# Optimization experiments

Hardware: AMD Instinct MI355X
Metric: run time of the kernel (lower is better)

The kernel has to match this reference:

```python
import jax, jax.numpy as jnp
import numpy as np

ALPHA = 0.5

def pairwise_sqdist(a, b):
    # a: [B,N,3], b: [B,M,3] -> [B,N,M] squared euclidean distances
    a2 = jnp.sum(a * a, axis=-1)[:, :, None]
    b2 = jnp.sum(b * b, axis=-1)[:, None, :]
    ab = jnp.einsum('bnd,bmd->bnm', a, b)
    return jnp.maximum(a2 + b2 - 2.0 * ab, 0.0)

def setup_inputs() -> dict:
    key = jax.random.key(0)
    k1, k2, k3, k4, k5 = jax.random.split(key, 5)
    B, N_UP, N_SEED, N_GT, N_RAD = 4, 8192, 2048, 8192, 1024
    return {
        'pc_up':   jax.random.normal(k1, (B, N_UP, 3), dtype=jnp.float32),
        'pc_seed': jax.random.normal(k2, (B, N_SEED, 3), dtype=jnp.float32),
        'pc_conf': jax.random.uniform(k3, (B, N_RAD, 1), dtype=jnp.float32),
        'pc2':     jax.random.normal(k4, (B, N_GT, 3), dtype=jnp.float32),
        'pc3':     jax.random.normal(k5, (B, N_RAD, 3), dtype=jnp.float32),
    }

def reference(pc_up, pc_seed, pc_conf, pc2, pc3):
    # --- confidence score target: exp(-min euclidean dist from radar to GT) ---
    d_rad_gt = pairwise_sqdist(pc3, pc2)                      # [B,N_rad,N_gt]
    min_dist = jnp.sqrt(jnp.min(d_rad_gt, axis=-1))           # [B,N_rad]
    gt_scores = jnp.exp(-min_dist)[..., None]                 # [B,N_rad,1]
    conf_loss = jnp.mean((pc_conf - gt_scores) ** 2)

    # --- Chamfer (squared distances, as standard ChamferDistance kernels) ---
    d_up_gt = pairwise_sqdist(pc_up, pc2)                     # [B,N_up,N_gt]
    dist1 = jnp.min(d_up_gt, axis=2)                          # up -> gt
    dist2 = jnp.min(d_up_gt, axis=1)                          # gt -> up
    chamfer_up = 0.5 * jnp.mean(dist1) + 2.0 * jnp.mean(dist2)

    # --- EMD surrogate: nearest-neighbor matching cost, sqrt(dist).mean() ---
    # (original uses an approximate auction-based emdFunction; nearest-neighbor
    # assignment is the standard differentiable reference surrogate)
    emd_loss = jnp.mean(jnp.sqrt(dist1))

    final_loss = ALPHA * chamfer_up + ALPHA * conf_loss + emd_loss
    return final_loss
```

## Files before the change

### kernel.cpp

```cpp
#include <hip/hip_runtime.h>
#include <math.h>


#define THREADS 256
#define NSPLIT 16
#define COLS 512
#define NTILES (COLS / 32)

typedef __attribute__((ext_vector_type(8))) short s8v;
typedef __attribute__((ext_vector_type(16))) float f16v;

__device__ __forceinline__ unsigned short f2bf(float x) {
    unsigned u = __float_as_uint(x);
    u += 0x7FFFu + ((u >> 16) & 1u);
    return (unsigned short)(u >> 16);
}
__device__ __forceinline__ float bf2f(unsigned short h) {
    return __uint_as_float((unsigned)h << 16);
}

__global__ __launch_bounds__(THREADS, 4) void
mfma_pass_kernel(const float* __restrict__ pc_up, const float* __restrict__ pc2,
                 const float* __restrict__ pc3,
                 float* p1, float* p2, float* p3) {
    __shared__ unsigned short tiles[NTILES][2][32][8];

    int bid = blockIdx.x;
    const float* Ap;
    const float* Bp;
    float* part;
    int NA, rowsTot;
    if (bid < 1024) {
        Ap = pc_up; Bp = pc2; part = p1; NA = 8192; rowsTot = 32768;
    } else if (bid < 2048) {
        bid -= 1024; Ap = pc2; Bp = pc_up; part = p2; NA = 8192; rowsTot = 32768;
    } else {
        bid -= 2048; Ap = pc3; Bp = pc2; part = p3; NA = 1024; rowsTot = 4096;
    }
    const int rb = bid >> 4, sp = bid & 15;
    const int NB = 8192;
    const int rowBase = rb * 512;
    const int batch = rowBase / NA;
    const int colBase = sp * COLS;

    const float* bsrc = Bp + ((size_t)batch * NB + colBase) * 3;
    for (int c = threadIdx.x; c < COLS; c += THREADS) {
        float x = bsrc[c * 3 + 0], y = bsrc[c * 3 + 1], z = bsrc[c * 3 + 2];
        float ux = -2.f * x, uy = -2.f * y, uz = -2.f * z;
        unsigned short uxh = f2bf(ux), uyh = f2bf(uy), uzh = f2bf(uz);
        unsigned short uxl = f2bf(ux - bf2f(uxh));
        unsigned short uyl = f2bf(uy - bf2f(uyh));
        unsigned short uzl = f2bf(uz - bf2f(uzh));
        float b2 = x * x + y * y + z * z;
        unsigned short b2h = f2bf(b2);
        unsigned short b2l = f2bf(b2 - bf2f(b2h));
        int ct = c >> 5, cc = c & 31;
        s8v h0 = {(short)uxh, (short)uyh, (short)uzh, (short)uxh,
                  (short)uyh, (short)uzh, (short)uxl, (short)uyl};
        s8v h1 = {(short)uzl, (short)b2h, (short)b2l, 0, 0, 0, 0, 0};
        *(s8v*)&tiles[ct][0][cc][0] = h0;
        *(s8v*)&tiles[ct][1][cc][0] = h1;
    }

    const int lane = threadIdx.x & 63;
    const int w = threadIdx.x >> 6;
    const int half = lane >> 5;
    const int rl = lane & 31;
    s8v afrag[4];
    float a2[4];
#pragma unroll
    for (int f = 0; f < 4; ++f) {
        int row = rowBase + (w * 4 + f) * 32 + rl;
        float x = Ap[row * 3 + 0], y = Ap[row * 3 + 1], z = Ap[row * 3 + 2];
        unsigned short xh = f2bf(x), yh = f2bf(y), zh = f2bf(z);
        unsigned short xl = f2bf(x - bf2f(xh));
        unsigned short yl = f2bf(y - bf2f(yh));
        unsigned short zl = f2bf(z - bf2f(zh));
        a2[f] = x * x + y * y + z * z;
        s8v fr0 = {(short)xh, (short)yh, (short)zh, (short)xl,
                   (short)yl, (short)zl, (short)xh, (short)yh};
        s8v fr1 = {(short)zh, (short)0x3F80, (short)0x3F80, 0, 0, 0, 0, 0};
        afrag[f] = half ? fr1 : fr0;
    }
    __syncthreads();

    f16v zero;
#pragma unroll
    for (int i = 0; i < 16; ++i) zero[i] = 0.0f;
    float m[4] = {INFINITY, INFINITY, INFINITY, INFINITY};

#pragma unroll 1
    for (int t = 0; t < NTILES; t += 2) {
        s8v b0 = *(const s8v*)&tiles[t + 0][half][rl][0];
        s8v b1 = *(const s8v*)&tiles[t + 1][half][rl][0];
#pragma unroll
        for (int f = 0; f < 4; ++f) {
            f16v d0 = __builtin_amdgcn_mfma_f32_32x32x16_bf16(
                b0, afrag[f], zero, 0, 0, 0);
            f16v d1 = __builtin_amdgcn_mfma_f32_32x32x16_bf16(
                b1, afrag[f], zero, 0, 0, 0);
            float u0 = fminf(fminf(d0[0], d0[1]), d0[2]);
            float u1 = fminf(fminf(d0[3], d0[4]), d0[5]);
            float u2 = fminf(fminf(d0[6], d0[7]), d0[8]);
            float u3 = fminf(fminf(d0[9], d0[10]), d0[11]);
            float u4 = fminf(fminf(d0[12], d0[13]), d0[14]);
            float v0 = fminf(fminf(u0, u1), u2);
            float v1 = fminf(fminf(u3, u4), d0[15]);
            float w0 = fminf(fminf(d1[0], d1[1]), d1[2]);
            float w1 = fminf(fminf(d1[3], d1[4]), d1[5]);
            float w2 = fminf(fminf(d1[6], d1[7]), d1[8]);
            float w3 = fminf(fminf(d1[9], d1[10]), d1[11]);
            float w4 = fminf(fminf(d1[12], d1[13]), d1[14]);
            float x0 = fminf(fminf(w0, w1), w2);
            float x1 = fminf(fminf(w3, w4), d1[15]);
            m[f] = fminf(m[f], fminf(fminf(v0, v1), fminf(x0, x1)));
        }
    }

#pragma unroll
    for (int f = 0; f < 4; ++f) {
        float v = fminf(m[f], __shfl_xor(m[f], 32, 64));
        float d = fmaxf(a2[f] + v, 0.0f);
        if (half == 0)
            part[sp * rowsTot + rowBase + (w * 4 + f) * 32 + rl] = d;
    }
}

__global__ __launch_bounds__(THREADS) void
reduce_kernel(const float* __restrict__ p1, const float* __restrict__ p2,
              const float* __restrict__ p3, const float* __restrict__ conf,
              float* __restrict__ out) {
    const int gid = blockIdx.x * THREADS + threadIdx.x;

    const float w1 = 0.25f / 32768.0f;
    const float wq = 1.0f / 32768.0f;
    const float w2 = 1.0f / 32768.0f;
    const float w3 = 0.5f / 4096.0f;

    float v1 = INFINITY, v2 = INFINITY;
#pragma unroll
    for (int sp = 0; sp < NSPLIT; ++sp) {
        v1 = fminf(v1, p1[sp * 32768 + gid]);
        v2 = fminf(v2, p2[sp * 32768 + gid]);
    }
    float s = w1 * v1 + wq * sqrtf(v1) + w2 * v2;
    if (gid < 4096) {
        float v3 = INFINITY;
#pragma unroll
        for (int sp = 0; sp < NSPLIT; ++sp)
            v3 = fminf(v3, p3[sp * 4096 + gid]);
        float diff = conf[gid] - expf(-sqrtf(v3));
        s += w3 * diff * diff;
    }

    __shared__ float wsum[4];
    const int lane = threadIdx.x & 63;
    const int wave = threadIdx.x >> 6;
    for (int off = 32; off > 0; off >>= 1) s += __shfl_down(s, off, 64);
    if (lane == 0) wsum[wave] = s;
    __syncthreads();
    if (threadIdx.x == 0)
        atomicAdd(out, wsum[0] + wsum[1] + wsum[2] + wsum[3]);
}

extern "C" void kernel_launch(void* const* d_in, const int* in_sizes, int n_in,
                              void* d_out, int out_size, void* d_ws, size_t ws_size,
                              hipStream_t stream) {
    const float* pc_up   = (const float*)d_in[0];
    const float* pc_conf = (const float*)d_in[2];
    const float* pc2     = (const float*)d_in[3];
    const float* pc3     = (const float*)d_in[4];

    float* p1 = (float*)d_ws;
    float* p2 = p1 + NSPLIT * 32768;
    float* p3 = p2 + NSPLIT * 32768;

    mfma_pass_kernel<<<2176, THREADS, 0, stream>>>(pc_up, pc2, pc3, p1, p2, p3);
    reduce_kernel<<<128, THREADS, 0, stream>>>(p1, p2, p3, pc_conf,
                                               (float*)d_out);
}
```

Before: 86.52 us.

## Retile to 256 rows by 1024 columns and defer the horizontal min reduction

Each block now covers 256 query rows against 1024 reference columns, with 8 column splits instead of 16, so each wave holds two A fragments instead of four. Inside the loop, the two MFMA outputs are folded elementwise into 16-wide min accumulators. The reduction across those 16 lanes happens once after the loop instead of on every iteration. The intent is fewer min instructions per MFMA and less partial-result traffic. In exchange, each block's B-tile LDS use doubles and each LDS tile read is reused by fewer MFMAs, which may lower occupancy.

```diff
diff --git a/kernel.cpp b/kernel.cpp
--- a/kernel.cpp
+++ b/kernel.cpp
@@ -3,8 +3,8 @@
 
 
 #define THREADS 256
-#define NSPLIT 16
-#define COLS 512
+#define NSPLIT 8
+#define COLS 1024
 #define NTILES (COLS / 32)
 
 typedef __attribute__((ext_vector_type(8))) short s8v;
@@ -37,9 +37,9 @@
     } else {
         bid -= 2048; Ap = pc3; Bp = pc2; part = p3; NA = 1024; rowsTot = 4096;
     }
-    const int rb = bid >> 4, sp = bid & 15;
+    const int rb = bid >> 3, sp = bid & 7;
     const int NB = 8192;
-    const int rowBase = rb * 512;
+    const int rowBase = rb * 256;
     const int batch = rowBase / NA;
     const int colBase = sp * COLS;
 
@@ -66,11 +66,11 @@
     const int w = threadIdx.x >> 6;
     const int half = lane >> 5;
     const int rl = lane & 31;
-    s8v afrag[4];
-    float a2[4];
+    s8v afrag[2];
+    float a2[2];
 #pragma unroll
-    for (int f = 0; f < 4; ++f) {
-        int row = rowBase + (w * 4 + f) * 32 + rl;
+    for (int f = 0; f < 2; ++f) {
+        int row = rowBase + (w * 2 + f) * 32 + rl;
         float x = Ap[row * 3 + 0], y = Ap[row * 3 + 1], z = Ap[row * 3 + 2];
         unsigned short xh = f2bf(x), yh = f2bf(y), zh = f2bf(z);
         unsigned short xl = f2bf(x - bf2f(xh));
@@ -87,42 +87,40 @@
     f16v zero;
 #pragma unroll
     for (int i = 0; i < 16; ++i) zero[i] = 0.0f;
-    float m[4] = {INFINITY, INFINITY, INFINITY, INFINITY};
+    f16v acc[2];
+#pragma unroll
+    for (int i = 0; i < 16; ++i) { acc[0][i] = INFINITY; acc[1][i] = INFINITY; }
 
 #pragma unroll 1
     for (int t = 0; t < NTILES; t += 2) {
         s8v b0 = *(const s8v*)&tiles[t + 0][half][rl][0];
         s8v b1 = *(const s8v*)&tiles[t + 1][half][rl][0];
 #pragma unroll
-        for (int f = 0; f < 4; ++f) {
+        for (int f = 0; f < 2; ++f) {
             f16v d0 = __builtin_amdgcn_mfma_f32_32x32x16_bf16(
                 b0, afrag[f], zero, 0, 0, 0);
             f16v d1 = __builtin_amdgcn_mfma_f32_32x32x16_bf16(
                 b1, afrag[f], zero, 0, 0, 0);
-            float u0 = fminf(fminf(d0[0], d0[1]), d0[2]);
-            float u1 = fminf(fminf(d0[3], d0[4]), d0[5]);
-            float u2 = fminf(fminf(d0[6], d0[7]), d0[8]);
-            float u3 = fminf(fminf(d0[9], d0[10]), d0[11]);
-            float u4 = fminf(fminf(d0[12], d0[13]), d0[14]);
-            float v0 = fminf(fminf(u0, u1), u2);
-            float v1 = fminf(fminf(u3, u4), d0[15]);
-            float w0 = fminf(fminf(d1[0], d1[1]), d1[2]);
-            float w1 = fminf(fminf(d1[3], d1[4]), d1[5]);
-            float w2 = fminf(fminf(d1[6], d1[7]), d1[8]);
-            float w3 = fminf(fminf(d1[9], d1[10]), d1[11]);
-            float w4 = fminf(fminf(d1[12], d1[13]), d1[14]);
-            float x0 = fminf(fminf(w0, w1), w2);
-            float x1 = fminf(fminf(w3, w4), d1[15]);
-            m[f] = fminf(m[f], fminf(fminf(v0, v1), fminf(x0, x1)));
+#pragma unroll
+            for (int i = 0; i < 16; ++i)
+                acc[f][i] = fminf(acc[f][i], fminf(d0[i], d1[i]));
         }
     }
 
 #pragma unroll
-    for (int f = 0; f < 4; ++f) {
-        float v = fminf(m[f], __shfl_xor(m[f], 32, 64));
+    for (int f = 0; f < 2; ++f) {
+        float u0 = fminf(fminf(acc[f][0], acc[f][1]), acc[f][2]);
+        float u1 = fminf(fminf(acc[f][3], acc[f][4]), acc[f][5]);
+        float u2 = fminf(fminf(acc[f][6], acc[f][7]), acc[f][8]);
+        float u3 = fminf(fminf(acc[f][9], acc[f][10]), acc[f][11]);
+        float u4 = fminf(fminf(acc[f][12], acc[f][13]), acc[f][14]);
+        float v0 = fminf(fminf(u0, u1), u2);
+        float v1 = fminf(fminf(u3, u4), acc[f][15]);
+        float m = fminf(v0, v1);
+        float v = fminf(m, __shfl_xor(m, 32, 64));
         float d = fmaxf(a2[f] + v, 0.0f);
         if (half == 0)
-            part[sp * rowsTot + rowBase + (w * 4 + f) * 32 + rl] = d;
+            part[sp * rowsTot + rowBase + (w * 2 + f) * 32 + rl] = d;
     }
 }
 
```

New measurement: 84.08 us. 1.03x faster.
